# Performance work log

Measured on AMD Instinct MI355X. Metric: run time of the kernel, lower is better.

Reference implementation:

```python
import jax, jax.numpy as jnp
import numpy as np

B, C, W, H, D = 4, 32, 64, 64, 64


def setup_inputs() -> dict:
    key = jax.random.key(0)
    ks = jax.random.split(key, 8)
    x = jax.random.normal(ks[0], (B, C, W, H, D), dtype=jnp.float32)
    # 1x1x1 Conv3d == per-voxel channel mixing: weight (C_out, C_in), bias (C_out,)
    Wq = jax.random.normal(ks[1], (C, C), dtype=jnp.float32) * 0.05
    bq = jax.random.normal(ks[2], (C,), dtype=jnp.float32) * 0.05
    Wk = jax.random.normal(ks[3], (C, C), dtype=jnp.float32) * 0.05
    bk = jax.random.normal(ks[4], (C,), dtype=jnp.float32) * 0.05
    Wv = jax.random.normal(ks[5], (C, C), dtype=jnp.float32) * 0.05
    bv = jax.random.normal(ks[6], (C,), dtype=jnp.float32) * 0.05
    gamma = jnp.float32(0.1)  # torch inits to 0; nonzero so output depends on attention
    return {"x": x, "Wq": Wq, "bq": bq, "Wk": Wk, "bk": bk, "Wv": Wv, "bv": bv, "gamma": gamma}


def reference(x, Wq, bq, Wk, bk, Wv, bv, gamma):
    b, c, w, h, d = x.shape
    N = w * h * d

    def proj(Wt, bt):
        # 1x1x1 conv then torch's .view(b, -1, c): a raw row-major reshape of
        # (b, c, w, h, d) -> (b, N, c) that interleaves channel/spatial (faithful).
        y = jnp.einsum('oc,bcwhd->bowhd', Wt, x) + bt[None, :, None, None, None]
        return y.reshape(b, N, c)

    q = proj(Wq, bq)  # (b, N, c)
    k = proj(Wk, bk)
    v = proj(Wv, bv)
    s = jnp.einsum('bnc,bnd->bcd', q, k)          # q^T k: tiny (b, c, c)
    a = jax.nn.softmax(s, axis=-1)
    scores = jnp.einsum('bnc,bcd->bnd', v, a)     # (b, N, c)
    return x + gamma * scores.reshape(b, c, w, h, d)
```

## Files before the change

kernel.cpp:

```cpp
#include <hip/hip_runtime.h>

typedef __attribute__((ext_vector_type(8))) short bf16x8;
typedef __attribute__((ext_vector_type(4))) float f32x4;

#define MSP   262144
#define BATCH 4
#define NT    8
#define NBLK  128

#define CSF   264
#define WTILE (8 * CSF)

#define OFF_P  0
#define OFF_CS 4096

#define GLDS16(gsrc, ldst)                                               \
  __builtin_amdgcn_global_load_lds(                                      \
      (const __attribute__((address_space(1))) unsigned int*)(gsrc),     \
      (__attribute__((address_space(3))) unsigned int*)(ldst), 16, 0, 0)

__device__ __forceinline__ unsigned short f2bf(float f) {
  unsigned int u = __float_as_uint(f);
  u += 0x7fffu + ((u >> 16) & 1u);
  return (unsigned short)(u >> 16);
}
__device__ __forceinline__ void split2(float f, short* hi, short* lo) {
  unsigned int u = __float_as_uint(f);
  unsigned int uh = u + (0x7fffu + ((u >> 16) & 1u));
  *hi = (short)(uh >> 16);
  const float r = f - __uint_as_float(uh & 0xffff0000u);
  *lo = (short)(__float_as_uint(r) >> 16);
}

#define MFMA(A, B, C) __builtin_amdgcn_mfma_f32_16x16x32_bf16(A, B, C, 0, 0, 0)


__global__ __launch_bounds__(256) void pass1_kernel(
    const float* __restrict__ x, const float* __restrict__ Wq,
    const float* __restrict__ Wk, float* __restrict__ ws) {
  __shared__ float XT[8 * WTILE];
  __shared__ float UW[3072];
  const int tid = threadIdx.x;
  const int w = tid >> 6, l = tid & 63, lm = tid & 15, lb = (tid >> 4) & 3;
  const int b = blockIdx.y;
  const size_t xbase = (size_t)b * 32 * MSP;
  const int wbase = (blockIdx.x * 4 + w) * (NT * 64);

  const int srow = l >> 4;
  const int scol = (l & 15) * 4;
  float* wbuf0 = XT + (w * 2 + 0) * WTILE;
  float* wbuf1 = XT + (w * 2 + 1) * WTILE;

#pragma unroll
  for (int c = 0; c < 8; ++c)
    GLDS16(x + xbase + (size_t)(c * 4 + srow) * MSP + wbase + scol,
           wbuf0 + c * CSF);

  {
    float* WqL = UW;
    float* WkL = UW + 1024;
    for (int k = tid; k < 1024; k += 256) { WqL[k] = Wq[k]; WkL[k] = Wk[k]; }
    __syncthreads();
    float* UL = UW + 2048;
    for (int k = tid; k < 1024; k += 256) {
      const int aa = k >> 5, bb = k & 31;
      float s = 0.f;
#pragma unroll
      for (int ch = 0; ch < 32; ++ch)
        s = fmaf(WqL[ch * 32 + aa], WkL[ch * 32 + bb], s);
      UL[k] = s;
    }
    __syncthreads();
  }
  bf16x8 uh0, ul0, uh1, ul1;
  {
    const float* UL = UW + 2048;
#pragma unroll
    for (int r = 0; r < 8; ++r) {
      const int kk = (r < 4) ? lb * 4 + r : 16 + lb * 4 + (r - 4);
      short h, lo;
      split2(UL[lm * 32 + kk], &h, &lo);        uh0[r] = h; ul0[r] = lo;
      split2(UL[(16 + lm) * 32 + kk], &h, &lo); uh1[r] = h; ul1[r] = lo;
    }
  }

  int ldsoff[8];
#pragma unroll
  for (int r = 0; r < 8; ++r) {
    const int ch = (r < 4) ? lb * 4 + r : 16 + lb * 4 + (r - 4);
    ldsoff[r] = (ch >> 2) * CSF + (ch & 3) * 64 + lm;
  }

  f32x4 p00 = {0, 0, 0, 0}, p01 = {0, 0, 0, 0}, p10 = {0, 0, 0, 0}, p11 = {0, 0, 0, 0};
  float cs0[8], cs1[8];
#pragma unroll
  for (int r = 0; r < 8; ++r) { cs0[r] = 0.f; cs1[r] = 0.f; }

#pragma unroll 1
  for (int t = 0; t < NT; ++t) {
    const float* XB = (t & 1) ? wbuf1 : wbuf0;
    float* XN = (t & 1) ? wbuf0 : wbuf1;
    if (t + 1 < NT) {
      const int posn = wbase + (t + 1) * 64;
#pragma unroll
      for (int c = 0; c < 8; ++c)
        GLDS16(x + xbase + (size_t)(c * 4 + srow) * MSP + posn + scol,
               XN + c * CSF);
      asm volatile("s_waitcnt vmcnt(8)" ::: "memory");
    } else {
      asm volatile("s_waitcnt vmcnt(0)" ::: "memory");
    }
    __builtin_amdgcn_sched_barrier(0);

#pragma unroll
    for (int g2 = 0; g2 < 2; ++g2) {
      const int pl = g2 * 32;
      float xf0[8], xf1[8];
#pragma unroll
      for (int r = 0; r < 8; ++r) {
        xf0[r] = XB[ldsoff[r] + pl];
        xf1[r] = XB[ldsoff[r] + pl + 16];
      }
      bf16x8 xh0, xl0, xh1, xl1;
#pragma unroll
      for (int r = 0; r < 8; ++r) {
        short h, lo;
        split2(xf0[r], &h, &lo); xh0[r] = h; xl0[r] = lo;
        split2(xf1[r], &h, &lo); xh1[r] = h; xl1[r] = lo;
        cs0[r] += xf0[r];  cs1[r] += xf1[r];
      }

      f32x4 y00 = {0,0,0,0}, y01 = {0,0,0,0}, y10 = {0,0,0,0}, y11 = {0,0,0,0};
      y00 = MFMA(uh0, xh0, y00); y00 = MFMA(uh0, xl0, y00); y00 = MFMA(ul0, xh0, y00);
      y01 = MFMA(uh1, xh0, y01); y01 = MFMA(uh1, xl0, y01); y01 = MFMA(ul1, xh0, y01);
      y10 = MFMA(uh0, xh1, y10); y10 = MFMA(uh0, xl1, y10); y10 = MFMA(ul0, xh1, y10);
      y11 = MFMA(uh1, xh1, y11); y11 = MFMA(uh1, xl1, y11); y11 = MFMA(ul1, xh1, y11);

      bf16x8 yh0, yl0, yh1, yl1;
#pragma unroll
      for (int r = 0; r < 4; ++r) {
        short h, lo;
        split2(y00[r], &h, &lo); yh0[r] = h; yl0[r] = lo;
        split2(y10[r], &h, &lo); yh1[r] = h; yl1[r] = lo;
      }
#pragma unroll
      for (int r = 4; r < 8; ++r) {
        short h, lo;
        split2(y01[r - 4], &h, &lo); yh0[r] = h; yl0[r] = lo;
        split2(y11[r - 4], &h, &lo); yh1[r] = h; yl1[r] = lo;
      }

      p00 = MFMA(xh0, yh0, p00); p00 = MFMA(xh0, yl0, p00); p00 = MFMA(xl0, yh0, p00);
      p01 = MFMA(xh0, yh1, p01); p01 = MFMA(xh0, yl1, p01); p01 = MFMA(xl0, yh1, p01);
      p10 = MFMA(xh1, yh0, p10); p10 = MFMA(xh1, yl0, p10); p10 = MFMA(xl1, yh0, p10);
      p11 = MFMA(xh1, yh1, p11); p11 = MFMA(xh1, yl1, p11); p11 = MFMA(xl1, yh1, p11);
    }
  }

  __syncthreads();
  float* red = XT;
#pragma unroll
  for (int r = 0; r < 4; ++r) {
    red[w * 1024 + (lb * 4 + r) * 32 + lm]           = p00[r];
    red[w * 1024 + (lb * 4 + r) * 32 + 16 + lm]      = p01[r];
    red[w * 1024 + (16 + lb * 4 + r) * 32 + lm]      = p10[r];
    red[w * 1024 + (16 + lb * 4 + r) * 32 + 16 + lm] = p11[r];
  }
  __syncthreads();
  for (int k = tid; k < 1024; k += 256) {
    const float s = red[k] + red[1024 + k] + red[2048 + k] + red[3072 + k];
    atomicAdd(&ws[OFF_P + b * 1024 + k], s);
  }
  __syncthreads();
#pragma unroll
  for (int r = 0; r < 8; ++r) {
    const int ch = (r < 4) ? lb * 4 + r : 16 + lb * 4 + (r - 4);
    red[w * 1024 + ch * 32 + lm]      = cs0[r];
    red[w * 1024 + ch * 32 + 16 + lm] = cs1[r];
  }
  __syncthreads();
  for (int k = tid; k < 1024; k += 256) {
    const float s = red[k] + red[1024 + k] + red[2048 + k] + red[3072 + k];
    atomicAdd(&ws[OFF_CS + b * 1024 + k], s);
  }
}

__global__ __launch_bounds__(256) void pass2_kernel(
    const float* __restrict__ x, const float* __restrict__ Wq,
    const float* __restrict__ bq, const float* __restrict__ Wk,
    const float* __restrict__ bk, const float* __restrict__ Wv,
    const float* __restrict__ bv, const float* __restrict__ gm,
    const float* __restrict__ ws, float* __restrict__ out) {
  __shared__ float XT[8 * WTILE];
  __shared__ float Sm[1024];
  __shared__ float u_l[32], v_l[32], su_l[32], sv_l[32], ca_l[32];
  __shared__ float beta_l;

  const int tid = threadIdx.x;
  const int w = tid >> 6, l = tid & 63, lm = tid & 15, lb = (tid >> 4) & 3;
  const int b = blockIdx.y;
  const size_t xbase = (size_t)b * 32 * MSP;
  const int wbase = (blockIdx.x * 4 + w) * (NT * 64);

  const int srow = l >> 4;
  const int scol = (l & 15) * 4;
  float* wbuf0 = XT + (w * 2 + 0) * WTILE;
  float* wbuf1 = XT + (w * 2 + 1) * WTILE;

#pragma unroll
  for (int c = 0; c < 8; ++c)
    GLDS16(x + xbase + (size_t)(c * 4 + srow) * MSP + wbase + scol,
           wbuf0 + c * CSF);

  if (tid < 32) {
    float u = 0.f;
#pragma unroll
    for (int ch = 0; ch < 32; ++ch) u = fmaf(Wq[ch * 32 + tid], bk[ch], u);
    u_l[tid] = u;
  } else if (tid < 64) {
    const int j = tid - 32;
    float v = 0.f;
#pragma unroll
    for (int ch = 0; ch < 32; ++ch) v = fmaf(bq[ch], Wk[ch * 32 + j], v);
    v_l[j] = v;
  } else if (tid == 64) {
    float bt = 0.f;
#pragma unroll
    for (int ch = 0; ch < 32; ++ch) bt = fmaf(bq[ch], bk[ch], bt);
    beta_l = bt;
  }
  __syncthreads();
  if (tid < 32) {
    float s = 0.f;
#pragma unroll
    for (int a = 0; a < 32; ++a)
      s = fmaf(u_l[a], ws[OFF_CS + b * 1024 + a * 32 + tid], s);
    su_l[tid] = s;
  } else if (tid < 64) {
    const int j = tid - 32;
    float s = 0.f;
#pragma unroll
    for (int a = 0; a < 32; ++a)
      s = fmaf(v_l[a], ws[OFF_CS + b * 1024 + a * 32 + j], s);
    sv_l[j] = s;
  }
  __syncthreads();
  {
    const int si = tid >> 3, sj0 = (tid & 7) * 4;
    float s4[4];
#pragma unroll
    for (int c = 0; c < 4; ++c)
      s4[c] = ws[OFF_P + b * 1024 + si * 32 + sj0 + c] + su_l[si] +
              sv_l[sj0 + c] + 8192.0f * beta_l;
    float mx = fmaxf(fmaxf(s4[0], s4[1]), fmaxf(s4[2], s4[3]));
    mx = fmaxf(mx, __shfl_xor(mx, 1, 8));
    mx = fmaxf(mx, __shfl_xor(mx, 2, 8));
    mx = fmaxf(mx, __shfl_xor(mx, 4, 8));
    float e4[4], sum = 0.f;
#pragma unroll
    for (int c = 0; c < 4; ++c) { e4[c] = expf(s4[c] - mx); sum += e4[c]; }
    sum += __shfl_xor(sum, 1, 8);
    sum += __shfl_xor(sum, 2, 8);
    sum += __shfl_xor(sum, 4, 8);
    const float inv = 1.0f / sum;
#pragma unroll
    for (int c = 0; c < 4; ++c) Sm[si * 32 + sj0 + c] = e4[c] * inv;
  }
  __syncthreads();
  if (tid < 32) {
    float c = 0.f;
#pragma unroll
    for (int ii = 0; ii < 32; ++ii) c += Sm[ii * 32 + tid];
    ca_l[tid] = c;
  }
  bf16x8 a0, a1, wv0, wv1;
#pragma unroll
  for (int r = 0; r < 8; ++r) {
    const int kk = (r < 4) ? lb * 4 + r : 16 + lb * 4 + (r - 4);
    a0[r]  = (short)f2bf(Sm[kk * 32 + lm]);
    a1[r]  = (short)f2bf(Sm[kk * 32 + 16 + lm]);
    wv0[r] = (short)f2bf(Wv[lm * 32 + kk]);
    wv1[r] = (short)f2bf(Wv[(16 + lm) * 32 + kk]);
  }
  __syncthreads();

  const float gamma = gm[0];
  const float bv0 = bv[lm], bv1 = bv[16 + lm];
  float i00[4], i01[4], i10[4], i11[4];
#pragma unroll
  for (int r = 0; r < 4; ++r) {
    const float c0 = ca_l[lb * 4 + r];
    const float c1 = ca_l[16 + lb * 4 + r];
    i00[r] = bv0 * c0; i01[r] = bv1 * c0;
    i10[r] = bv0 * c1; i11[r] = bv1 * c1;
  }

  int ldsoff[8];
#pragma unroll
  for (int r = 0; r < 8; ++r) {
    const int ch = (r < 4) ? lb * 4 + r : 16 + lb * 4 + (r - 4);
    ldsoff[r] = (ch >> 2) * CSF + (ch & 3) * 64 + lm;
  }
  int resoff[2][2];
#pragma unroll
  for (int CT = 0; CT < 2; ++CT)
#pragma unroll
    for (int MT = 0; MT < 2; ++MT)
      resoff[CT][MT] = (CT * 4 + (lm >> 2)) * CSF + (lm & 3) * 64 +
                       MT * 16 + lb * 4;

#pragma unroll 1
  for (int t = 0; t < NT; ++t) {
    const float* XB = (t & 1) ? wbuf1 : wbuf0;
    float* XN = (t & 1) ? wbuf0 : wbuf1;
    if (t + 1 < NT) {
      const int posn = wbase + (t + 1) * 64;
#pragma unroll
      for (int c = 0; c < 8; ++c)
        GLDS16(x + xbase + (size_t)(c * 4 + srow) * MSP + posn + scol,
               XN + c * CSF);
      if (t == 0)
        asm volatile("s_waitcnt vmcnt(8)" ::: "memory");
      else
        asm volatile("s_waitcnt vmcnt(16)" ::: "memory");
    } else {
      asm volatile("s_waitcnt vmcnt(8)" ::: "memory");
    }
    __builtin_amdgcn_sched_barrier(0);
    const int post = wbase + t * 64;

#pragma unroll
    for (int g2 = 0; g2 < 2; ++g2) {
      const int pl = g2 * 32;
      bf16x8 xh0, xh1;
#pragma unroll
      for (int r = 0; r < 8; ++r) {
        xh0[r] = (short)f2bf(XB[ldsoff[r] + pl]);
        xh1[r] = (short)f2bf(XB[ldsoff[r] + pl + 16]);
      }
      f32x4 v00 = {0,0,0,0}, v01 = {0,0,0,0}, v10 = {0,0,0,0}, v11 = {0,0,0,0};
      v00 = MFMA(xh0, wv0, v00); v01 = MFMA(xh0, wv1, v01);
      v10 = MFMA(xh1, wv0, v10); v11 = MFMA(xh1, wv1, v11);

      bf16x8 vb0, vb1;
#pragma unroll
      for (int r = 0; r < 4; ++r) { vb0[r] = (short)f2bf(v00[r]); vb1[r] = (short)f2bf(v01[r]); }
#pragma unroll
      for (int r = 4; r < 8; ++r) { vb0[r] = (short)f2bf(v10[r - 4]); vb1[r] = (short)f2bf(v11[r - 4]); }

      f32x4 t00 = {i00[0], i00[1], i00[2], i00[3]};
      f32x4 t01 = {i01[0], i01[1], i01[2], i01[3]};
      f32x4 t10 = {i10[0], i10[1], i10[2], i10[3]};
      f32x4 t11 = {i11[0], i11[1], i11[2], i11[3]};
      t00 = MFMA(a0, vb0, t00); t01 = MFMA(a0, vb1, t01);
      t10 = MFMA(a1, vb0, t10); t11 = MFMA(a1, vb1, t11);

#define EPI(TT, MT, CT)                                                           \
      {                                                                           \
        const f32x4 xr = *reinterpret_cast<const f32x4*>(&XB[resoff[CT][MT] + pl]); \
        const size_t addr = xbase + (size_t)((CT) * 16 + lm) * MSP +              \
                            (size_t)(post + pl + (MT) * 16 + lb * 4);             \
        f32x4 o;                                                                  \
        o[0] = fmaf(gamma, TT[0], xr[0]); o[1] = fmaf(gamma, TT[1], xr[1]);       \
        o[2] = fmaf(gamma, TT[2], xr[2]); o[3] = fmaf(gamma, TT[3], xr[3]);       \
        *reinterpret_cast<f32x4*>(out + addr) = o;                                \
      }
      EPI(t00, 0, 0); EPI(t01, 0, 1); EPI(t10, 1, 0); EPI(t11, 1, 1);
#undef EPI
    }
  }
}

extern "C" void kernel_launch(void* const* d_in, const int* in_sizes, int n_in,
                              void* d_out, int out_size, void* d_ws, size_t ws_size,
                              hipStream_t stream) {
  const float* x  = (const float*)d_in[0];
  const float* Wq = (const float*)d_in[1];
  const float* bq = (const float*)d_in[2];
  const float* Wk = (const float*)d_in[3];
  const float* bk = (const float*)d_in[4];
  const float* Wv = (const float*)d_in[5];
  const float* bv = (const float*)d_in[6];
  const float* gm = (const float*)d_in[7];
  float* out = (float*)d_out;
  float* ws  = (float*)d_ws;

  hipMemsetAsync(ws, 0, 8192 * sizeof(float), stream);
  pass1_kernel<<<dim3(NBLK, BATCH), 256, 0, stream>>>(x, Wq, Wk, ws);
  pass2_kernel<<<dim3(NBLK, BATCH), 256, 0, stream>>>(x, Wq, bq, Wk, bk, Wv, bv,
                                                      gm, ws, out);
}
```

Measured before the change: 82.53 us.

## Halve per-step tiles, double blocks, swizzle LDS staging, add MFMA priority

Each wave now stages 32 positions per step instead of 64, using half the LDS per block and launching twice as many blocks. Staging rows hold 8 channels with a rotated column swizzle, so the fragment and residual LDS reads avoid bank conflicts. Pass 1 computes Wq^T·Wk straight from global memory instead of copying both into LDS first. s_setprio wraps the MFMA sections. The smaller tiles raise occupancy and parallelism but add per-iteration loop and wait overhead.

After: 89.56 us. +8.5%, slower.

```diff
diff --git a/kernel.cpp b/kernel.cpp
--- a/kernel.cpp
+++ b/kernel.cpp
@@ -6,10 +6,10 @@
 #define MSP   262144
 #define BATCH 4
 #define NT    8
-#define NBLK  128
-
-#define CSF   264
-#define WTILE (8 * CSF)
+#define NBLK  256
+
+#define CSF2  264
+#define WT2   (4 * CSF2)
 
 #define OFF_P  0
 #define OFF_CS 4096
@@ -38,57 +38,54 @@
 __global__ __launch_bounds__(256) void pass1_kernel(
     const float* __restrict__ x, const float* __restrict__ Wq,
     const float* __restrict__ Wk, float* __restrict__ ws) {
-  __shared__ float XT[8 * WTILE];
-  __shared__ float UW[3072];
+  __shared__ __align__(16) float XT[8 * WT2];
+  __shared__ float UL[1024];
   const int tid = threadIdx.x;
   const int w = tid >> 6, l = tid & 63, lm = tid & 15, lb = (tid >> 4) & 3;
   const int b = blockIdx.y;
   const size_t xbase = (size_t)b * 32 * MSP;
-  const int wbase = (blockIdx.x * 4 + w) * (NT * 64);
-
-  const int srow = l >> 4;
-  const int scol = (l & 15) * 4;
-  float* wbuf0 = XT + (w * 2 + 0) * WTILE;
-  float* wbuf1 = XT + (w * 2 + 1) * WTILE;
-
-#pragma unroll
-  for (int c = 0; c < 8; ++c)
-    GLDS16(x + xbase + (size_t)(c * 4 + srow) * MSP + wbase + scol,
-           wbuf0 + c * CSF);
-
-  {
-    float* WqL = UW;
-    float* WkL = UW + 1024;
-    for (int k = tid; k < 1024; k += 256) { WqL[k] = Wq[k]; WkL[k] = Wk[k]; }
-    __syncthreads();
-    float* UL = UW + 2048;
-    for (int k = tid; k < 1024; k += 256) {
-      const int aa = k >> 5, bb = k & 31;
-      float s = 0.f;
-#pragma unroll
-      for (int ch = 0; ch < 32; ++ch)
-        s = fmaf(WqL[ch * 32 + aa], WkL[ch * 32 + bb], s);
-      UL[k] = s;
-    }
-    __syncthreads();
-  }
+  const int wbase = (blockIdx.x * 4 + w) * (NT * 32);
+
+  const int srow = l >> 3;
+  const int scol = (((l & 7) + srow) & 7) * 4;
+  float* wbuf0 = XT + (w * 2 + 0) * WT2;
+  float* wbuf1 = XT + (w * 2 + 1) * WT2;
+  const float* csrc[4];
+#pragma unroll
+  for (int c = 0; c < 4; ++c)
+    csrc[c] = x + xbase + (size_t)(c * 8 + srow) * MSP + scol;
+
+#pragma unroll
+  for (int c = 0; c < 4; ++c)
+    GLDS16(csrc[c] + wbase, wbuf0 + c * CSF2);
+
+  for (int k = tid; k < 1024; k += 256) {
+    const int aa = k >> 5, bb = k & 31;
+    float s = 0.f;
+#pragma unroll
+    for (int ch = 0; ch < 32; ++ch)
+      s = fmaf(Wq[ch * 32 + aa], Wk[ch * 32 + bb], s);
+    UL[k] = s;
+  }
+  __syncthreads();
+
   bf16x8 uh0, ul0, uh1, ul1;
-  {
-    const float* UL = UW + 2048;
-#pragma unroll
-    for (int r = 0; r < 8; ++r) {
-      const int kk = (r < 4) ? lb * 4 + r : 16 + lb * 4 + (r - 4);
-      short h, lo;
-      split2(UL[lm * 32 + kk], &h, &lo);        uh0[r] = h; ul0[r] = lo;
-      split2(UL[(16 + lm) * 32 + kk], &h, &lo); uh1[r] = h; ul1[r] = lo;
-    }
-  }
-
-  int ldsoff[8];
+#pragma unroll
+  for (int r = 0; r < 8; ++r) {
+    const int kk = (r < 4) ? lb * 4 + r : 16 + lb * 4 + (r - 4);
+    short h, lo;
+    split2(UL[lm * 32 + kk], &h, &lo);        uh0[r] = h; ul0[r] = lo;
+    split2(UL[(16 + lm) * 32 + kk], &h, &lo); uh1[r] = h; ul1[r] = lo;
+  }
+
+  int off0[8], off1[8];
 #pragma unroll
   for (int r = 0; r < 8; ++r) {
     const int ch = (r < 4) ? lb * 4 + r : 16 + lb * 4 + (r - 4);
-    ldsoff[r] = (ch >> 2) * CSF + (ch & 3) * 64 + lm;
+    const int base = (ch >> 3) * CSF2 + (ch & 7) * 32 + (lm & 3);
+    const int g0 = ((lm >> 2) - (ch & 7)) & 7;
+    off0[r] = base + g0 * 4;
+    off1[r] = base + ((g0 + 4) & 7) * 4;
   }
 
   f32x4 p00 = {0, 0, 0, 0}, p01 = {0, 0, 0, 0}, p10 = {0, 0, 0, 0}, p11 = {0, 0, 0, 0};
@@ -101,60 +98,54 @@
     const float* XB = (t & 1) ? wbuf1 : wbuf0;
     float* XN = (t & 1) ? wbuf0 : wbuf1;
     if (t + 1 < NT) {
-      const int posn = wbase + (t + 1) * 64;
-#pragma unroll
-      for (int c = 0; c < 8; ++c)
-        GLDS16(x + xbase + (size_t)(c * 4 + srow) * MSP + posn + scol,
-               XN + c * CSF);
-      asm volatile("s_waitcnt vmcnt(8)" ::: "memory");
+      const int posn = wbase + (t + 1) * 32;
+#pragma unroll
+      for (int c = 0; c < 4; ++c)
+        GLDS16(csrc[c] + posn, XN + c * CSF2);
+      asm volatile("s_waitcnt vmcnt(4)" ::: "memory");
     } else {
       asm volatile("s_waitcnt vmcnt(0)" ::: "memory");
     }
     __builtin_amdgcn_sched_barrier(0);
 
-#pragma unroll
-    for (int g2 = 0; g2 < 2; ++g2) {
-      const int pl = g2 * 32;
-      float xf0[8], xf1[8];
-#pragma unroll
-      for (int r = 0; r < 8; ++r) {
-        xf0[r] = XB[ldsoff[r] + pl];
-        xf1[r] = XB[ldsoff[r] + pl + 16];
-      }
-      bf16x8 xh0, xl0, xh1, xl1;
-#pragma unroll
-      for (int r = 0; r < 8; ++r) {
-        short h, lo;
-        split2(xf0[r], &h, &lo); xh0[r] = h; xl0[r] = lo;
-        split2(xf1[r], &h, &lo); xh1[r] = h; xl1[r] = lo;
-        cs0[r] += xf0[r];  cs1[r] += xf1[r];
-      }
-
-      f32x4 y00 = {0,0,0,0}, y01 = {0,0,0,0}, y10 = {0,0,0,0}, y11 = {0,0,0,0};
-      y00 = MFMA(uh0, xh0, y00); y00 = MFMA(uh0, xl0, y00); y00 = MFMA(ul0, xh0, y00);
-      y01 = MFMA(uh1, xh0, y01); y01 = MFMA(uh1, xl0, y01); y01 = MFMA(ul1, xh0, y01);
-      y10 = MFMA(uh0, xh1, y10); y10 = MFMA(uh0, xl1, y10); y10 = MFMA(ul0, xh1, y10);
-      y11 = MFMA(uh1, xh1, y11); y11 = MFMA(uh1, xl1, y11); y11 = MFMA(ul1, xh1, y11);
-
-      bf16x8 yh0, yl0, yh1, yl1;
-#pragma unroll
-      for (int r = 0; r < 4; ++r) {
-        short h, lo;
-        split2(y00[r], &h, &lo); yh0[r] = h; yl0[r] = lo;
-        split2(y10[r], &h, &lo); yh1[r] = h; yl1[r] = lo;
-      }
-#pragma unroll
-      for (int r = 4; r < 8; ++r) {
-        short h, lo;
-        split2(y01[r - 4], &h, &lo); yh0[r] = h; yl0[r] = lo;
-        split2(y11[r - 4], &h, &lo); yh1[r] = h; yl1[r] = lo;
-      }
-
-      p00 = MFMA(xh0, yh0, p00); p00 = MFMA(xh0, yl0, p00); p00 = MFMA(xl0, yh0, p00);
-      p01 = MFMA(xh0, yh1, p01); p01 = MFMA(xh0, yl1, p01); p01 = MFMA(xl0, yh1, p01);
-      p10 = MFMA(xh1, yh0, p10); p10 = MFMA(xh1, yl0, p10); p10 = MFMA(xl1, yh0, p10);
-      p11 = MFMA(xh1, yh1, p11); p11 = MFMA(xh1, yl1, p11); p11 = MFMA(xl1, yh1, p11);
-    }
+    float xf0[8], xf1[8];
+#pragma unroll
+    for (int r = 0; r < 8; ++r) { xf0[r] = XB[off0[r]]; xf1[r] = XB[off1[r]]; }
+    bf16x8 xh0, xl0, xh1, xl1;
+#pragma unroll
+    for (int r = 0; r < 8; ++r) {
+      short h, lo;
+      split2(xf0[r], &h, &lo); xh0[r] = h; xl0[r] = lo;
+      split2(xf1[r], &h, &lo); xh1[r] = h; xl1[r] = lo;
+      cs0[r] += xf0[r];  cs1[r] += xf1[r];
+    }
+
+    __builtin_amdgcn_s_setprio(1);
+    f32x4 y00 = {0,0,0,0}, y01 = {0,0,0,0}, y10 = {0,0,0,0}, y11 = {0,0,0,0};
+    y00 = MFMA(uh0, xh0, y00); y00 = MFMA(uh0, xl0, y00); y00 = MFMA(ul0, xh0, y00);
+    y01 = MFMA(uh1, xh0, y01); y01 = MFMA(uh1, xl0, y01); y01 = MFMA(ul1, xh0, y01);
+    y10 = MFMA(uh0, xh1, y10); y10 = MFMA(uh0, xl1, y10); y10 = MFMA(ul0, xh1, y10);
+    y11 = MFMA(uh1, xh1, y11); y11 = MFMA(uh1, xl1, y11); y11 = MFMA(ul1, xh1, y11);
+
+    bf16x8 yh0, yl0, yh1, yl1;
+#pragma unroll
+    for (int r = 0; r < 4; ++r) {
+      short h, lo;
+      split2(y00[r], &h, &lo); yh0[r] = h; yl0[r] = lo;
+      split2(y10[r], &h, &lo); yh1[r] = h; yl1[r] = lo;
+    }
+#pragma unroll
+    for (int r = 4; r < 8; ++r) {
+      short h, lo;
+      split2(y01[r - 4], &h, &lo); yh0[r] = h; yl0[r] = lo;
+      split2(y11[r - 4], &h, &lo); yh1[r] = h; yl1[r] = lo;
+    }
+
+    p00 = MFMA(xh0, yh0, p00); p00 = MFMA(xh0, yl0, p00); p00 = MFMA(xl0, yh0, p00);
+    p01 = MFMA(xh0, yh1, p01); p01 = MFMA(xh0, yl1, p01); p01 = MFMA(xl0, yh1, p01);
+    p10 = MFMA(xh1, yh0, p10); p10 = MFMA(xh1, yl0, p10); p10 = MFMA(xl1, yh0, p10);
+    p11 = MFMA(xh1, yh1, p11); p11 = MFMA(xh1, yl1, p11); p11 = MFMA(xl1, yh1, p11);
+    __builtin_amdgcn_s_setprio(0);
   }
 
   __syncthreads();
@@ -191,7 +182,7 @@
     const float* __restrict__ bk, const float* __restrict__ Wv,
     const float* __restrict__ bv, const float* __restrict__ gm,
     const float* __restrict__ ws, float* __restrict__ out) {
-  __shared__ float XT[8 * WTILE];
+  __shared__ __align__(16) float XT[8 * WT2];
   __shared__ float Sm[1024];
   __shared__ float u_l[32], v_l[32], su_l[32], sv_l[32], ca_l[32];
   __shared__ float beta_l;
@@ -200,17 +191,20 @@
   const int w = tid >> 6, l = tid & 63, lm = tid & 15, lb = (tid >> 4) & 3;
   const int b = blockIdx.y;
   const size_t xbase = (size_t)b * 32 * MSP;
-  const int wbase = (blockIdx.x * 4 + w) * (NT * 64);
-
-  const int srow = l >> 4;
-  const int scol = (l & 15) * 4;
-  float* wbuf0 = XT + (w * 2 + 0) * WTILE;
-  float* wbuf1 = XT + (w * 2 + 1) * WTILE;
-
-#pragma unroll
-  for (int c = 0; c < 8; ++c)
-    GLDS16(x + xbase + (size_t)(c * 4 + srow) * MSP + wbase + scol,
-           wbuf0 + c * CSF);
+  const int wbase = (blockIdx.x * 4 + w) * (NT * 32);
+
+  const int srow = l >> 3;
+  const int scol = (((l & 7) + srow) & 7) * 4;
+  float* wbuf0 = XT + (w * 2 + 0) * WT2;
+  float* wbuf1 = XT + (w * 2 + 1) * WT2;
+  const float* csrc[4];
+#pragma unroll
+  for (int c = 0; c < 4; ++c)
+    csrc[c] = x + xbase + (size_t)(c * 8 + srow) * MSP + scol;
+
+#pragma unroll
+  for (int c = 0; c < 4; ++c)
+    GLDS16(csrc[c] + wbase, wbuf0 + c * CSF2);
 
   if (tid < 32) {
     float u = 0.f;
@@ -295,79 +289,76 @@
     i10[r] = bv0 * c1; i11[r] = bv1 * c1;
   }
 
-  int ldsoff[8];
+  int off0[8], off1[8];
 #pragma unroll
   for (int r = 0; r < 8; ++r) {
     const int ch = (r < 4) ? lb * 4 + r : 16 + lb * 4 + (r - 4);
-    ldsoff[r] = (ch >> 2) * CSF + (ch & 3) * 64 + lm;
-  }
-  int resoff[2][2];
+    const int base = (ch >> 3) * CSF2 + (ch & 7) * 32 + (lm & 3);
+    const int g0 = ((lm >> 2) - (ch & 7)) & 7;
+    off0[r] = base + g0 * 4;
+    off1[r] = base + ((g0 + 4) & 7) * 4;
+  }
+  int res[2][2];
 #pragma unroll
   for (int CT = 0; CT < 2; ++CT)
 #pragma unroll
     for (int MT = 0; MT < 2; ++MT)
-      resoff[CT][MT] = (CT * 4 + (lm >> 2)) * CSF + (lm & 3) * 64 +
-                       MT * 16 + lb * 4;
+      res[CT][MT] = (CT * 2 + (lm >> 3)) * CSF2 + (lm & 7) * 32 +
+                    4 * ((MT * 4 + lb - (lm & 7)) & 7);
 
 #pragma unroll 1
   for (int t = 0; t < NT; ++t) {
     const float* XB = (t & 1) ? wbuf1 : wbuf0;
     float* XN = (t & 1) ? wbuf0 : wbuf1;
     if (t + 1 < NT) {
-      const int posn = wbase + (t + 1) * 64;
-#pragma unroll
-      for (int c = 0; c < 8; ++c)
-        GLDS16(x + xbase + (size_t)(c * 4 + srow) * MSP + posn + scol,
-               XN + c * CSF);
-      if (t == 0)
-        asm volatile("s_waitcnt vmcnt(8)" ::: "memory");
-      else
-        asm volatile("s_waitcnt vmcnt(16)" ::: "memory");
+      const int posn = wbase + (t + 1) * 32;
+#pragma unroll
+      for (int c = 0; c < 4; ++c)
+        GLDS16(csrc[c] + posn, XN + c * CSF2);
+      asm volatile("s_waitcnt vmcnt(8)" ::: "memory");
     } else {
-      asm volatile("s_waitcnt vmcnt(8)" ::: "memory");
+      asm volatile("s_waitcnt vmcnt(4)" ::: "memory");
     }
     __builtin_amdgcn_sched_barrier(0);
-    const int post = wbase + t * 64;
-
-#pragma unroll
-    for (int g2 = 0; g2 < 2; ++g2) {
-      const int pl = g2 * 32;
-      bf16x8 xh0, xh1;
-#pragma unroll
-      for (int r = 0; r < 8; ++r) {
-        xh0[r] = (short)f2bf(XB[ldsoff[r] + pl]);
-        xh1[r] = (short)f2bf(XB[ldsoff[r] + pl + 16]);
-      }
-      f32x4 v00 = {0,0,0,0}, v01 = {0,0,0,0}, v10 = {0,0,0,0}, v11 = {0,0,0,0};
-      v00 = MFMA(xh0, wv0, v00); v01 = MFMA(xh0, wv1, v01);
-      v10 = MFMA(xh1, wv0, v10); v11 = MFMA(xh1, wv1, v11);
-
-      bf16x8 vb0, vb1;
-#pragma unroll
-      for (int r = 0; r < 4; ++r) { vb0[r] = (short)f2bf(v00[r]); vb1[r] = (short)f2bf(v01[r]); }
-#pragma unroll
-      for (int r = 4; r < 8; ++r) { vb0[r] = (short)f2bf(v10[r - 4]); vb1[r] = (short)f2bf(v11[r - 4]); }
-
-      f32x4 t00 = {i00[0], i00[1], i00[2], i00[3]};
-      f32x4 t01 = {i01[0], i01[1], i01[2], i01[3]};
-      f32x4 t10 = {i10[0], i10[1], i10[2], i10[3]};
-      f32x4 t11 = {i11[0], i11[1], i11[2], i11[3]};
-      t00 = MFMA(a0, vb0, t00); t01 = MFMA(a0, vb1, t01);
-      t10 = MFMA(a1, vb0, t10); t11 = MFMA(a1, vb1, t11);
+    const int post = wbase + t * 32;
+
+    bf16x8 xh0, xh1;
+#pragma unroll
+    for (int r = 0; r < 8; ++r) {
+      xh0[r] = (short)f2bf(XB[off0[r]]);
+      xh1[r] = (short)f2bf(XB[off1[r]]);
+    }
+    __builtin_amdgcn_s_setprio(1);
+    f32x4 v00 = {0,0,0,0}, v01 = {0,0,0,0}, v10 = {0,0,0,0}, v11 = {0,0,0,0};
+    v00 = MFMA(xh0, wv0, v00); v01 = MFMA(xh0, wv1, v01);
+    v10 = MFMA(xh1, wv0, v10); v11 = MFMA(xh1, wv1, v11);
+
+    bf16x8 vb0, vb1;
+#pragma unroll
+    for (int r = 0; r < 4; ++r) { vb0[r] = (short)f2bf(v00[r]); vb1[r] = (short)f2bf(v01[r]); }
+#pragma unroll
+    for (int r = 4; r < 8; ++r) { vb0[r] = (short)f2bf(v10[r - 4]); vb1[r] = (short)f2bf(v11[r - 4]); }
+
+    f32x4 t00 = {i00[0], i00[1], i00[2], i00[3]};
+    f32x4 t01 = {i01[0], i01[1], i01[2], i01[3]};
+    f32x4 t10 = {i10[0], i10[1], i10[2], i10[3]};
+    f32x4 t11 = {i11[0], i11[1], i11[2], i11[3]};
+    t00 = MFMA(a0, vb0, t00); t01 = MFMA(a0, vb1, t01);
+    t10 = MFMA(a1, vb0, t10); t11 = MFMA(a1, vb1, t11);
+    __builtin_amdgcn_s_setprio(0);
 
 #define EPI(TT, MT, CT)                                                           \
-      {                                                                           \
-        const f32x4 xr = *reinterpret_cast<const f32x4*>(&XB[resoff[CT][MT] + pl]); \
-        const size_t addr = xbase + (size_t)((CT) * 16 + lm) * MSP +              \
-                            (size_t)(post + pl + (MT) * 16 + lb * 4);             \
-        f32x4 o;                                                                  \
-        o[0] = fmaf(gamma, TT[0], xr[0]); o[1] = fmaf(gamma, TT[1], xr[1]);       \
-        o[2] = fmaf(gamma, TT[2], xr[2]); o[3] = fmaf(gamma, TT[3], xr[3]);       \
-        *reinterpret_cast<f32x4*>(out + addr) = o;                                \
-      }
-      EPI(t00, 0, 0); EPI(t01, 0, 1); EPI(t10, 1, 0); EPI(t11, 1, 1);
+    {                                                                             \
+      const f32x4 xr = *reinterpret_cast<const f32x4*>(&XB[res[CT][MT]]);         \
+      const size_t addr = xbase + (size_t)((CT) * 16 + lm) * MSP +                \
+                          (size_t)(post + (MT) * 16 + lb * 4);                    \
+      f32x4 o;                                                                    \
+      o[0] = fmaf(gamma, TT[0], xr[0]); o[1] = fmaf(gamma, TT[1], xr[1]);         \
+      o[2] = fmaf(gamma, TT[2], xr[2]); o[3] = fmaf(gamma, TT[3], xr[3]);         \
+      *reinterpret_cast<f32x4*>(out + addr) = o;                                  \
+    }
+    EPI(t00, 0, 0); EPI(t01, 0, 1); EPI(t10, 1, 0); EPI(t11, 1, 1);
 #undef EPI
-    }
   }
 }
 
```
